# Kernel tuning notes

Measured on AMD Instinct MI355X. Metric: run time of the kernel, lower is better.

## Reference

```python
import jax, jax.numpy as jnp
import numpy as np

B, S, D = 1, 2048, 1024
NH, NKV, HD = 16, 4, 64
N_REP = NH // NKV


def _rope_tables(seq_len, half_dim, base=10000.0):
    inv_freq = 1.0 / (base ** (np.arange(0, half_dim, dtype=np.float32) / half_dim))
    t = np.arange(seq_len, dtype=np.float32)
    freqs = np.outer(t, inv_freq)  # (S, HD//2)
    return jnp.asarray(np.cos(freqs)), jnp.asarray(np.sin(freqs))


def setup_inputs() -> dict:
    key = jax.random.key(0)
    ks = jax.random.split(key, 5)
    x = jax.random.normal(ks[0], (B, S, D), dtype=jnp.float32)
    rope_cos, rope_sin = _rope_tables(S, HD // 2)
    sd = 1.0 / np.sqrt(D)
    Wq = jax.random.normal(ks[1], (D, NH * HD), dtype=jnp.float32) * sd
    Wk = jax.random.normal(ks[2], (D, NKV * HD), dtype=jnp.float32) * sd
    Wv = jax.random.normal(ks[3], (D, NKV * HD), dtype=jnp.float32) * sd
    Wo = jax.random.normal(ks[4], (NH * HD, D), dtype=jnp.float32) * sd
    return {"x": x, "rope_cos": rope_cos, "rope_sin": rope_sin,
            "Wq": Wq, "Wk": Wk, "Wv": Wv, "Wo": Wo}


def _apply_rope(t, cos, sin):
    # t: (B, H, S, HD); cos/sin: (S, HD//2). Rotate-half convention.
    t1, t2 = jnp.split(t, 2, axis=-1)
    c = cos[None, None, :, :]
    s = sin[None, None, :, :]
    return jnp.concatenate([t1 * c - t2 * s, t2 * c + t1 * s], axis=-1)


def reference(x, rope_cos, rope_sin, Wq, Wk, Wv, Wo):
    b, s, _ = x.shape
    # projections -> (B, H, S, HD)
    q = (x @ Wq).reshape(b, s, NH, HD).transpose(0, 2, 1, 3)
    k = (x @ Wk).reshape(b, s, NKV, HD).transpose(0, 2, 1, 3)
    v = (x @ Wv).reshape(b, s, NKV, HD).transpose(0, 2, 1, 3)
    q = _apply_rope(q, rope_cos, rope_sin)
    k = _apply_rope(k, rope_cos, rope_sin)
    # GQA expansion (repeat_interleave on head axis)
    k = jnp.repeat(k, N_REP, axis=1)
    v = jnp.repeat(v, N_REP, axis=1)
    scale = HD ** -0.5
    scores = jnp.einsum('bhqd,bhkd->bhqk', q, k) * scale
    causal = jnp.tril(jnp.ones((s, s), dtype=bool))
    scores = jnp.where(causal[None, None], scores, jnp.float32(-jnp.inf))
    attn = jax.nn.softmax(scores, axis=-1)
    out = jnp.einsum('bhqk,bhkd->bhqd', attn, v)  # (B, H, S, HD)
    out = out.transpose(0, 2, 1, 3).reshape(b, s, NH * HD)
    return out @ Wo
```

## Files before the change

kernel.cpp:

```cpp
#include <hip/hip_runtime.h>

typedef unsigned short ushort_t;
typedef __attribute__((ext_vector_type(8))) short short8;
typedef __attribute__((ext_vector_type(4))) float f32x4;
typedef __attribute__((ext_vector_type(4))) unsigned short ushort4v;
typedef __attribute__((ext_vector_type(8))) unsigned short ushort8v;

#define S_LEN 2048
#define D_MODEL 1024
#define NH 16
#define NKV 4
#define HD 64

__device__ __forceinline__ ushort_t f2bf(float f) {
    unsigned u = __float_as_uint(f);
    u += 0x7fffu + ((u >> 16) & 1u);
    return (ushort_t)(u >> 16);
}

__device__ __forceinline__ void cp16(void* lds, const void* g) {
    __builtin_amdgcn_global_load_lds(
        (__attribute__((address_space(1))) void*)g,
        (__attribute__((address_space(3))) void*)lds, 16, 0, 0);
}

__global__ __launch_bounds__(256) void prep_kernel(
    const float* __restrict__ x, ushort_t* __restrict__ xb,
    const float* __restrict__ Wq, const float* __restrict__ Wk,
    const float* __restrict__ Wv, const float* __restrict__ Wo,
    ushort_t* __restrict__ WqT, ushort_t* __restrict__ WkT,
    ushort_t* __restrict__ WvT, ushort_t* __restrict__ WoT)
{
    const int t = threadIdx.x;
    if (blockIdx.z == 4) {
        const int b  = blockIdx.y * 16 + blockIdx.x;
        const int i0 = (b * 256 + t) * 4;
        #pragma unroll
        for (int rep = 0; rep < 8; ++rep) {
            const int i = i0 + rep * 262144;
            float4 v = *(const float4*)(x + i);
            ushort4v o = { f2bf(v.x), f2bf(v.y), f2bf(v.z), f2bf(v.w) };
            *(ushort4v*)(xb + i) = o;
        }
        return;
    }
    __shared__ ushort_t T[64 * 72];
    const float* W; ushort_t* WT; int N;
    switch (blockIdx.z) {
        case 0:  W = Wq; WT = WqT; N = 1024; break;
        case 1:  W = Wk; WT = WkT; N = 256;  break;
        case 2:  W = Wv; WT = WvT; N = 256;  break;
        default: W = Wo; WT = WoT; N = 1024; break;
    }
    const int n0 = blockIdx.y * 64;
    if (n0 >= N) return;
    const int k0 = blockIdx.x * 64;
    const int kr = t >> 4, nc = (t & 15) * 4;
    #pragma unroll
    for (int p = 0; p < 4; ++p) {
        const int k = kr + p * 16;
        float4 v = *(const float4*)(W + (size_t)(k0 + k) * N + n0 + nc);
        T[(nc + 0) * 72 + k] = f2bf(v.x);
        T[(nc + 1) * 72 + k] = f2bf(v.y);
        T[(nc + 2) * 72 + k] = f2bf(v.z);
        T[(nc + 3) * 72 + k] = f2bf(v.w);
    }
    __syncthreads();
    const int n = t >> 2, seg = (t & 3) * 16;
    ushort8v a = *(ushort8v*)&T[n * 72 + seg];
    ushort8v b = *(ushort8v*)&T[n * 72 + seg + 8];
    *(ushort8v*)(WT + (size_t)(n0 + n) * 1024 + k0 + seg)     = a;
    *(ushort8v*)(WT + (size_t)(n0 + n) * 1024 + k0 + seg + 8) = b;
}

__global__ __launch_bounds__(256, 2) void gemm_qkv_mfma(
    const ushort_t* __restrict__ xb, const ushort_t* __restrict__ WqT,
    const ushort_t* __restrict__ WkT, const ushort_t* __restrict__ WvT,
    const float* __restrict__ rc, const float* __restrict__ rs,
    ushort_t* __restrict__ Qb, ushort_t* __restrict__ Kb,
    ushort_t* __restrict__ Vtb)
{
    __shared__ ushort_t As[2][64 * 64];
    __shared__ ushort_t Bs[2][128 * 64];

    const int t = threadIdx.x;
    const int lane = t & 63, wave = t >> 6;
    const int wr = wave >> 1, wc = wave & 1;
    const int quad = lane >> 4, l15 = lane & 15;
    const int lq = lane >> 3, lr = lane & 7;
    const int swz_st = (lr ^ lq) * 8;
    const int l7 = l15 & 7;
    const int fsw0 = (quad ^ l7) * 8;
    const int fsw1 = ((quad + 4) ^ l7) * 8;

    const int m0 = blockIdx.x * 64;
    const int cy = blockIdx.y;

    const ushort_t* WT; int nloc;
    if (cy < 8)       { WT = WqT; nloc = cy * 128; }
    else if (cy < 10) { WT = WkT; nloc = (cy - 8) * 128; }
    else              { WT = WvT; nloc = (cy - 10) * 128; }

    f32x4 acc[2][4];
    #pragma unroll
    for (int i = 0; i < 2; ++i)
        #pragma unroll
        for (int j = 0; j < 4; ++j) acc[i][j] = (f32x4)0.f;

    auto stage = [&](int buf, int k0) {
        #pragma unroll
        for (int i = 0; i < 2; ++i) {
            const int r = wave * 16 + i * 8 + lq;
            cp16(&As[buf][(wave * 16 + i * 8) * 64],
                 xb + (size_t)(m0 + r) * 1024 + k0 + swz_st);
        }
        #pragma unroll
        for (int i = 0; i < 4; ++i) {
            const int r = wave * 32 + i * 8 + lq;
            cp16(&Bs[buf][(wave * 32 + i * 8) * 64],
                 WT + (size_t)(nloc + r) * 1024 + k0 + swz_st);
        }
    };

    stage(0, 0);
    __syncthreads();

    for (int kk = 0; kk < 16; ++kk) {
        const int cur = kk & 1;
        if (kk + 1 < 16) stage(cur ^ 1, (kk + 1) * 64);

        const ushort_t* Ac = &As[cur][0];
        const ushort_t* Bc = &Bs[cur][0];
        #pragma unroll
        for (int hh = 0; hh < 2; ++hh) {
            const int fsw = hh ? fsw1 : fsw0;
            short8 av[2], bv[4];
            #pragma unroll
            for (int i = 0; i < 2; ++i)
                av[i] = *(const short8*)&Ac[(wr * 32 + i * 16 + l15) * 64 + fsw];
            #pragma unroll
            for (int j = 0; j < 4; ++j)
                bv[j] = *(const short8*)&Bc[(wc * 64 + j * 16 + l15) * 64 + fsw];
            #pragma unroll
            for (int i = 0; i < 2; ++i)
                #pragma unroll
                for (int j = 0; j < 4; ++j)
                    acc[i][j] = __builtin_amdgcn_mfma_f32_16x16x32_bf16(
                        av[i], bv[j], acc[i][j], 0, 0, 0);
        }
        __syncthreads();
    }

    if (cy < 10) {
        ushort_t* dst = (cy < 8) ? Qb : Kb;
        const float qs = (cy < 8) ? 0.125f : 1.0f;
        const int h = ((cy < 8) ? cy : (cy - 8)) * 2 + wc;
        #pragma unroll
        for (int i = 0; i < 2; ++i) {
            #pragma unroll
            for (int j = 0; j < 2; ++j) {
                const int d = j * 16 + l15;
                #pragma unroll
                for (int reg = 0; reg < 4; ++reg) {
                    const int s = m0 + wr * 32 + i * 16 + quad * 4 + reg;
                    const float c  = rc[s * 32 + d];
                    const float sn = rs[s * 32 + d];
                    const float v1 = acc[i][j][reg];
                    const float v2 = acc[i][j + 2][reg];
                    dst[((size_t)h * S_LEN + s) * HD + d]      = f2bf((v1 * c - v2 * sn) * qs);
                    dst[((size_t)h * S_LEN + s) * HD + d + 32] = f2bf((v2 * c + v1 * sn) * qs);
                }
            }
        }
    } else {
        const int vh = (cy - 10) * 2 + wc;
        #pragma unroll
        for (int i = 0; i < 2; ++i) {
            const int s0 = m0 + wr * 32 + i * 16 + quad * 4;
            #pragma unroll
            for (int j = 0; j < 4; ++j) {
                const int d = j * 16 + l15;
                ushort4v o = { f2bf(acc[i][j][0]), f2bf(acc[i][j][1]),
                               f2bf(acc[i][j][2]), f2bf(acc[i][j][3]) };
                *(ushort4v*)&Vtb[((size_t)vh * HD + d) * S_LEN + s0] = o;
            }
        }
    }
}

__global__ __launch_bounds__(128, 2) void attn_mfma(
    const ushort_t* __restrict__ Qb, const ushort_t* __restrict__ Kb,
    const ushort_t* __restrict__ Vtb, ushort_t* __restrict__ attnb)
{
    __shared__ ushort_t Ks[2][2][64 * 64];
    __shared__ ushort_t Vs[2][2][64 * 64];
    __shared__ ushort_t Ps[2][32 * 64];

    const int t = threadIdx.x;
    const int lane = t & 63, wave = t >> 6;
    const int quad = lane >> 4, l15 = lane & 15;
    const int lq = lane >> 3, lr = lane & 7;
    const int swz_st = (lr ^ lq) * 8;
    const int l7 = l15 & 7;
    const int fsw0 = (quad ^ l7) * 8;
    const int fsw1 = ((quad + 4) ^ l7) * 8;

    const int h  = blockIdx.x;
    const int y  = blockIdx.y;
    const int qt = (y < 16) ? y : 47 - y;
    const int q0 = qt * 64;
    const int kvh = h >> 2;
    const int wrow0 = q0 + wave * 32;

    const ushort_t* Qg = Qb + ((size_t)h * S_LEN + wrow0) * HD;
    const ushort_t* Kg = Kb + (size_t)kvh * S_LEN * HD;
    const ushort_t* Vg = Vtb + (size_t)kvh * HD * S_LEN;

    short8 aq[2][2];
    #pragma unroll
    for (int i = 0; i < 2; ++i) {
        aq[i][0] = *(const short8*)(Qg + (size_t)(i * 16 + l15) * HD + quad * 8);
        aq[i][1] = *(const short8*)(Qg + (size_t)(i * 16 + l15) * HD + 32 + quad * 8);
    }

    float ps[2][4];
    f32x4 Oacc[2][4];
    #pragma unroll
    for (int i = 0; i < 2; ++i)
        #pragma unroll
        for (int jb = 0; jb < 4; ++jb) { Oacc[i][jb] = (f32x4)0.f; ps[i][jb] = 0.f; }

    const int nround = (qt + 2) >> 1;

    auto stage = [&](int buf, int kvbase) {
        #pragma unroll
        for (int u = 0; u < 2; ++u)
            #pragma unroll
            for (int i = 0; i < 4; ++i) {
                const int r = wave * 32 + i * 8 + lq;
                cp16(&Ks[buf][u][(wave * 32 + i * 8) * 64],
                     Kg + (size_t)(kvbase + u * 64 + r) * 64 + swz_st);
                cp16(&Vs[buf][u][(wave * 32 + i * 8) * 64],
                     Vg + (size_t)r * 2048 + kvbase + u * 64 + swz_st);
            }
    };

    stage(0, 0);
    __syncthreads();

    ushort_t* Pw = &Ps[wave][0];

    for (int round = 0; round < nround; ++round) {
        const int cur = round & 1;
        if (round + 1 < nround) stage(cur ^ 1, (round + 1) * 128);

        #pragma unroll
        for (int u = 0; u < 2; ++u) {
            const int kv0 = round * 128 + u * 64;
            if (kv0 > q0 + 63) break;
            const ushort_t* Kc = &Ks[cur][u][0];
            const ushort_t* Vc = &Vs[cur][u][0];

            f32x4 sv[2][4];
            #pragma unroll
            for (int jb = 0; jb < 4; ++jb) {
                short8 b0 = *(const short8*)&Kc[(jb * 16 + l15) * 64 + fsw0];
                short8 b1 = *(const short8*)&Kc[(jb * 16 + l15) * 64 + fsw1];
                #pragma unroll
                for (int i = 0; i < 2; ++i) {
                    f32x4 z = (f32x4)0.f;
                    z = __builtin_amdgcn_mfma_f32_16x16x32_bf16(aq[i][0], b0, z, 0, 0, 0);
                    z = __builtin_amdgcn_mfma_f32_16x16x32_bf16(aq[i][1], b1, z, 0, 0, 0);
                    sv[i][jb] = z;
                }
            }

            const bool diag = (kv0 == q0);
            #pragma unroll
            for (int i = 0; i < 2; ++i)
                #pragma unroll
                for (int jb = 0; jb < 4; ++jb) {
                    const int col = kv0 + jb * 16 + l15;
                    #pragma unroll
                    for (int reg = 0; reg < 4; ++reg) {
                        float e = __expf(sv[i][jb][reg]);
                        if (diag && col > wrow0 + i * 16 + quad * 4 + reg) e = 0.f;
                        sv[i][jb][reg] = e;
                        ps[i][reg] += e;
                    }
                }

            #pragma unroll
            for (int i = 0; i < 2; ++i)
                #pragma unroll
                for (int jb = 0; jb < 4; ++jb)
                    #pragma unroll
                    for (int reg = 0; reg < 4; ++reg) {
                        const int row = i * 16 + quad * 4 + reg;
                        const int seg = (jb * 2 + (l15 >> 3)) ^ (row & 7);
                        Pw[row * 64 + seg * 8 + (l15 & 7)] =
                            (ushort_t)(__float_as_uint(sv[i][jb][reg]) >> 16);
                    }

            short8 pf[2][2];
            #pragma unroll
            for (int i = 0; i < 2; ++i) {
                pf[i][0] = *(const short8*)&Pw[(i * 16 + l15) * 64 + fsw0];
                pf[i][1] = *(const short8*)&Pw[(i * 16 + l15) * 64 + fsw1];
            }

            #pragma unroll
            for (int jb = 0; jb < 4; ++jb) {
                short8 v0 = *(const short8*)&Vc[(jb * 16 + l15) * 64 + fsw0];
                short8 v1 = *(const short8*)&Vc[(jb * 16 + l15) * 64 + fsw1];
                #pragma unroll
                for (int i = 0; i < 2; ++i) {
                    Oacc[i][jb] = __builtin_amdgcn_mfma_f32_16x16x32_bf16(
                        pf[i][0], v0, Oacc[i][jb], 0, 0, 0);
                    Oacc[i][jb] = __builtin_amdgcn_mfma_f32_16x16x32_bf16(
                        pf[i][1], v1, Oacc[i][jb], 0, 0, 0);
                }
            }
        }

        __syncthreads();
    }

    #pragma unroll
    for (int i = 0; i < 2; ++i)
        #pragma unroll
        for (int reg = 0; reg < 4; ++reg) {
            float l = ps[i][reg];
            l += __shfl_xor(l, 1);
            l += __shfl_xor(l, 2);
            l += __shfl_xor(l, 4);
            l += __shfl_xor(l, 8);
            const float inv = 1.f / l;
            const int s = wrow0 + i * 16 + quad * 4 + reg;
            #pragma unroll
            for (int jb = 0; jb < 4; ++jb)
                attnb[(size_t)s * D_MODEL + h * HD + jb * 16 + l15] =
                    f2bf(Oacc[i][jb][reg] * inv);
        }
}

__global__ __launch_bounds__(256, 2) void gemm_out_mfma(
    const ushort_t* __restrict__ Ab, const ushort_t* __restrict__ WoT,
    float* __restrict__ out)
{
    __shared__ ushort_t As[2][64 * 64];
    __shared__ ushort_t Bs[2][64 * 64];

    const int t = threadIdx.x;
    const int lane = t & 63, wave = t >> 6;
    const int wr = wave >> 1, wc = wave & 1;
    const int quad = lane >> 4, l15 = lane & 15;
    const int lq = lane >> 3, lr = lane & 7;
    const int swz_st = (lr ^ lq) * 8;
    const int l7 = l15 & 7;
    const int fsw0 = (quad ^ l7) * 8;
    const int fsw1 = ((quad + 4) ^ l7) * 8;

    const int m0 = blockIdx.x * 64;
    const int n0 = blockIdx.y * 64;

    f32x4 acc[2][2];
    #pragma unroll
    for (int i = 0; i < 2; ++i)
        #pragma unroll
        for (int j = 0; j < 2; ++j) acc[i][j] = (f32x4)0.f;

    auto stage = [&](int buf, int k0) {
        #pragma unroll
        for (int i = 0; i < 2; ++i) {
            const int r = wave * 16 + i * 8 + lq;
            cp16(&As[buf][(wave * 16 + i * 8) * 64],
                 Ab + (size_t)(m0 + r) * 1024 + k0 + swz_st);
            cp16(&Bs[buf][(wave * 16 + i * 8) * 64],
                 WoT + (size_t)(n0 + r) * 1024 + k0 + swz_st);
        }
    };

    stage(0, 0);
    __syncthreads();

    for (int kk = 0; kk < 16; ++kk) {
        const int cur = kk & 1;
        if (kk + 1 < 16) stage(cur ^ 1, (kk + 1) * 64);

        const ushort_t* Ac = &As[cur][0];
        const ushort_t* Bc = &Bs[cur][0];
        #pragma unroll
        for (int hh = 0; hh < 2; ++hh) {
            const int fsw = hh ? fsw1 : fsw0;
            short8 av[2], bv[2];
            #pragma unroll
            for (int i = 0; i < 2; ++i)
                av[i] = *(const short8*)&Ac[(wr * 32 + i * 16 + l15) * 64 + fsw];
            #pragma unroll
            for (int j = 0; j < 2; ++j)
                bv[j] = *(const short8*)&Bc[(wc * 32 + j * 16 + l15) * 64 + fsw];
            #pragma unroll
            for (int i = 0; i < 2; ++i)
                #pragma unroll
                for (int j = 0; j < 2; ++j)
                    acc[i][j] = __builtin_amdgcn_mfma_f32_16x16x32_bf16(
                        av[i], bv[j], acc[i][j], 0, 0, 0);
        }
        __syncthreads();
    }

    #pragma unroll
    for (int i = 0; i < 2; ++i)
        #pragma unroll
        for (int reg = 0; reg < 4; ++reg) {
            const int s = m0 + wr * 32 + i * 16 + quad * 4 + reg;
            #pragma unroll
            for (int j = 0; j < 2; ++j)
                out[(size_t)s * D_MODEL + n0 + wc * 32 + j * 16 + l15] = acc[i][j][reg];
        }
}

extern "C" void kernel_launch(void* const* d_in, const int* in_sizes, int n_in,
                              void* d_out, int out_size, void* d_ws, size_t ws_size,
                              hipStream_t stream)
{
    const float* x  = (const float*)d_in[0];
    const float* rc = (const float*)d_in[1];
    const float* rs = (const float*)d_in[2];
    const float* Wq = (const float*)d_in[3];
    const float* Wk = (const float*)d_in[4];
    const float* Wv = (const float*)d_in[5];
    const float* Wo = (const float*)d_in[6];
    float* out = (float*)d_out;

    ushort_t* xb   = (ushort_t*)d_ws;
    ushort_t* WqT  = xb   + (size_t)2048 * 1024;
    ushort_t* WkT  = WqT  + (size_t)1024 * 1024;
    ushort_t* WvT  = WkT  + (size_t)256 * 1024;
    ushort_t* WoT  = WvT  + (size_t)256 * 1024;
    ushort_t* Qb   = WoT  + (size_t)1024 * 1024;
    ushort_t* Kb   = Qb   + (size_t)NH * S_LEN * HD;
    ushort_t* Vtb  = Kb   + (size_t)NKV * S_LEN * HD;
    ushort_t* attnb= Vtb  + (size_t)NKV * HD * S_LEN;

    prep_kernel<<<dim3(16, 16, 5), 256, 0, stream>>>(x, xb, Wq, Wk, Wv, Wo,
                                                     WqT, WkT, WvT, WoT);
    gemm_qkv_mfma<<<dim3(32, 12), 256, 0, stream>>>(xb, WqT, WkT, WvT,
                                                    rc, rs, Qb, Kb, Vtb);
    attn_mfma<<<dim3(NH, 32), 128, 0, stream>>>(Qb, Kb, Vtb, attnb);
    gemm_out_mfma<<<dim3(32, 16), 256, 0, stream>>>(attnb, WoT, out);
}
```

Baseline: 154.4 us.

## Split causal attention along KV into partial blocks and add combine kernel

Attention work is now split along the KV axis (split-K / flash-decoding style). Each query tile is divided into up to four chunks of eight 64-wide KV tiles, giving 80×16 blocks with bounded work, launched longest-first. Partial unnormalized outputs and row sums are written in fp32 to a workspace, and a new combine kernel sums them, normalizes and converts to bf16. The goal is to balance the causal triangle's uneven load across CUs. The cost is extra fp32 global traffic, an extra kernel launch, and single-tile staging in place of 128-wide double tiles.

Result: faster. 146.5 us (-5.1%).

```diff
diff --git a/kernel.cpp b/kernel.cpp
--- a/kernel.cpp
+++ b/kernel.cpp
@@ -190,10 +190,11 @@
 
 __global__ __launch_bounds__(128, 2) void attn_mfma(
     const ushort_t* __restrict__ Qb, const ushort_t* __restrict__ Kb,
-    const ushort_t* __restrict__ Vtb, ushort_t* __restrict__ attnb)
-{
-    __shared__ ushort_t Ks[2][2][64 * 64];
-    __shared__ ushort_t Vs[2][2][64 * 64];
+    const ushort_t* __restrict__ Vtb, float* __restrict__ Opart,
+    float* __restrict__ lpart)
+{
+    __shared__ ushort_t Ks[2][64 * 64];
+    __shared__ ushort_t Vs[2][64 * 64];
     __shared__ ushort_t Ps[2][32 * 64];
 
     const int t = threadIdx.x;
@@ -205,10 +206,18 @@
     const int fsw0 = (quad ^ l7) * 8;
     const int fsw1 = ((quad + 4) ^ l7) * 8;
 
-    const int h  = blockIdx.x;
-    const int y  = blockIdx.y;
-    const int qt = (y < 16) ? y : 47 - y;
-    const int q0 = qt * 64;
+    const int x = 79 - blockIdx.x;
+    int qt, k;
+    if (x < 8)       { qt = x;               k = 0; }
+    else if (x < 24) { qt = 8 + (x - 8) / 2;  k = (x - 8) & 1; }
+    else if (x < 48) { qt = 16 + (x - 24) / 3; k = (x - 24) % 3; }
+    else             { qt = 24 + (x - 48) / 4; k = (x - 48) & 3; }
+    const int start = k * 8;
+    const int end   = min(start + 8, qt + 1);
+    const int nsub  = end - start;
+
+    const int h   = blockIdx.y;
+    const int q0  = qt * 64;
     const int kvh = h >> 2;
     const int wrow0 = q0 + wave * 32;
 
@@ -230,102 +239,98 @@
         #pragma unroll
         for (int jb = 0; jb < 4; ++jb) { Oacc[i][jb] = (f32x4)0.f; ps[i][jb] = 0.f; }
 
-    const int nround = (qt + 2) >> 1;
-
-    auto stage = [&](int buf, int kvbase) {
-        #pragma unroll
-        for (int u = 0; u < 2; ++u)
-            #pragma unroll
-            for (int i = 0; i < 4; ++i) {
-                const int r = wave * 32 + i * 8 + lq;
-                cp16(&Ks[buf][u][(wave * 32 + i * 8) * 64],
-                     Kg + (size_t)(kvbase + u * 64 + r) * 64 + swz_st);
-                cp16(&Vs[buf][u][(wave * 32 + i * 8) * 64],
-                     Vg + (size_t)r * 2048 + kvbase + u * 64 + swz_st);
+    auto stage = [&](int buf, int kvt) {
+        const int kvbase = kvt * 64;
+        #pragma unroll
+        for (int i = 0; i < 4; ++i) {
+            const int r = wave * 32 + i * 8 + lq;
+            cp16(&Ks[buf][(wave * 32 + i * 8) * 64],
+                 Kg + (size_t)(kvbase + r) * 64 + swz_st);
+            cp16(&Vs[buf][(wave * 32 + i * 8) * 64],
+                 Vg + (size_t)r * 2048 + kvbase + swz_st);
+        }
+    };
+
+    stage(0, start);
+    __syncthreads();
+
+    ushort_t* Pw = &Ps[wave][0];
+
+    for (int ssub = 0; ssub < nsub; ++ssub) {
+        const int cur = ssub & 1;
+        if (ssub + 1 < nsub) stage(cur ^ 1, start + ssub + 1);
+
+        const int kvt = start + ssub;
+        const int kv0 = kvt * 64;
+        const ushort_t* Kc = &Ks[cur][0];
+        const ushort_t* Vc = &Vs[cur][0];
+
+        f32x4 sv[2][4];
+        #pragma unroll
+        for (int jb = 0; jb < 4; ++jb) {
+            short8 b0 = *(const short8*)&Kc[(jb * 16 + l15) * 64 + fsw0];
+            short8 b1 = *(const short8*)&Kc[(jb * 16 + l15) * 64 + fsw1];
+            #pragma unroll
+            for (int i = 0; i < 2; ++i) {
+                f32x4 z = (f32x4)0.f;
+                z = __builtin_amdgcn_mfma_f32_16x16x32_bf16(aq[i][0], b0, z, 0, 0, 0);
+                z = __builtin_amdgcn_mfma_f32_16x16x32_bf16(aq[i][1], b1, z, 0, 0, 0);
+                sv[i][jb] = z;
             }
-    };
-
-    stage(0, 0);
-    __syncthreads();
-
-    ushort_t* Pw = &Ps[wave][0];
-
-    for (int round = 0; round < nround; ++round) {
-        const int cur = round & 1;
-        if (round + 1 < nround) stage(cur ^ 1, (round + 1) * 128);
-
-        #pragma unroll
-        for (int u = 0; u < 2; ++u) {
-            const int kv0 = round * 128 + u * 64;
-            if (kv0 > q0 + 63) break;
-            const ushort_t* Kc = &Ks[cur][u][0];
-            const ushort_t* Vc = &Vs[cur][u][0];
-
-            f32x4 sv[2][4];
+        }
+
+        const bool diag = (kvt == qt);
+        #pragma unroll
+        for (int i = 0; i < 2; ++i)
             #pragma unroll
             for (int jb = 0; jb < 4; ++jb) {
-                short8 b0 = *(const short8*)&Kc[(jb * 16 + l15) * 64 + fsw0];
-                short8 b1 = *(const short8*)&Kc[(jb * 16 + l15) * 64 + fsw1];
+                const int col = kv0 + jb * 16 + l15;
                 #pragma unroll
-                for (int i = 0; i < 2; ++i) {
-                    f32x4 z = (f32x4)0.f;
-                    z = __builtin_amdgcn_mfma_f32_16x16x32_bf16(aq[i][0], b0, z, 0, 0, 0);
-                    z = __builtin_amdgcn_mfma_f32_16x16x32_bf16(aq[i][1], b1, z, 0, 0, 0);
-                    sv[i][jb] = z;
+                for (int reg = 0; reg < 4; ++reg) {
+                    float e = __expf(sv[i][jb][reg]);
+                    if (diag && col > wrow0 + i * 16 + quad * 4 + reg) e = 0.f;
+                    sv[i][jb][reg] = e;
+                    ps[i][reg] += e;
                 }
             }
 
-            const bool diag = (kv0 == q0);
-            #pragma unroll
-            for (int i = 0; i < 2; ++i)
+        #pragma unroll
+        for (int i = 0; i < 2; ++i)
+            #pragma unroll
+            for (int jb = 0; jb < 4; ++jb)
                 #pragma unroll
-                for (int jb = 0; jb < 4; ++jb) {
-                    const int col = kv0 + jb * 16 + l15;
-                    #pragma unroll
-                    for (int reg = 0; reg < 4; ++reg) {
-                        float e = __expf(sv[i][jb][reg]);
-                        if (diag && col > wrow0 + i * 16 + quad * 4 + reg) e = 0.f;
-                        sv[i][jb][reg] = e;
-                        ps[i][reg] += e;
-                    }
+                for (int reg = 0; reg < 4; ++reg) {
+                    const int row = i * 16 + quad * 4 + reg;
+                    const int seg = (jb * 2 + (l15 >> 3)) ^ (row & 7);
+                    Pw[row * 64 + seg * 8 + (l15 & 7)] =
+                        (ushort_t)(__float_as_uint(sv[i][jb][reg]) >> 16);
                 }
 
-            #pragma unroll
-            for (int i = 0; i < 2; ++i)
-                #pragma unroll
-                for (int jb = 0; jb < 4; ++jb)
-                    #pragma unroll
-                    for (int reg = 0; reg < 4; ++reg) {
-                        const int row = i * 16 + quad * 4 + reg;
-                        const int seg = (jb * 2 + (l15 >> 3)) ^ (row & 7);
-                        Pw[row * 64 + seg * 8 + (l15 & 7)] =
-                            (ushort_t)(__float_as_uint(sv[i][jb][reg]) >> 16);
-                    }
-
-            short8 pf[2][2];
+        short8 pf[2][2];
+        #pragma unroll
+        for (int i = 0; i < 2; ++i) {
+            pf[i][0] = *(const short8*)&Pw[(i * 16 + l15) * 64 + fsw0];
+            pf[i][1] = *(const short8*)&Pw[(i * 16 + l15) * 64 + fsw1];
+        }
+
+        #pragma unroll
+        for (int jb = 0; jb < 4; ++jb) {
+            short8 v0 = *(const short8*)&Vc[(jb * 16 + l15) * 64 + fsw0];
+            short8 v1 = *(const short8*)&Vc[(jb * 16 + l15) * 64 + fsw1];
             #pragma unroll
             for (int i = 0; i < 2; ++i) {
-                pf[i][0] = *(const short8*)&Pw[(i * 16 + l15) * 64 + fsw0];
-                pf[i][1] = *(const short8*)&Pw[(i * 16 + l15) * 64 + fsw1];
+                Oacc[i][jb] = __builtin_amdgcn_mfma_f32_16x16x32_bf16(
+                    pf[i][0], v0, Oacc[i][jb], 0, 0, 0);
+                Oacc[i][jb] = __builtin_amdgcn_mfma_f32_16x16x32_bf16(
+                    pf[i][1], v1, Oacc[i][jb], 0, 0, 0);
             }
-
-            #pragma unroll
-            for (int jb = 0; jb < 4; ++jb) {
-                short8 v0 = *(const short8*)&Vc[(jb * 16 + l15) * 64 + fsw0];
-                short8 v1 = *(const short8*)&Vc[(jb * 16 + l15) * 64 + fsw1];
-                #pragma unroll
-                for (int i = 0; i < 2; ++i) {
-                    Oacc[i][jb] = __builtin_amdgcn_mfma_f32_16x16x32_bf16(
-                        pf[i][0], v0, Oacc[i][jb], 0, 0, 0);
-                    Oacc[i][jb] = __builtin_amdgcn_mfma_f32_16x16x32_bf16(
-                        pf[i][1], v1, Oacc[i][jb], 0, 0, 0);
-                }
-            }
         }
 
         __syncthreads();
     }
 
+    float* Op = Opart + (size_t)k * S_LEN * D_MODEL;
+    float* lp = lpart + (size_t)k * S_LEN * NH;
     #pragma unroll
     for (int i = 0; i < 2; ++i)
         #pragma unroll
@@ -335,13 +340,36 @@
             l += __shfl_xor(l, 2);
             l += __shfl_xor(l, 4);
             l += __shfl_xor(l, 8);
-            const float inv = 1.f / l;
             const int s = wrow0 + i * 16 + quad * 4 + reg;
+            if (l15 == 0) lp[s * NH + h] = l;
             #pragma unroll
             for (int jb = 0; jb < 4; ++jb)
-                attnb[(size_t)s * D_MODEL + h * HD + jb * 16 + l15] =
-                    f2bf(Oacc[i][jb][reg] * inv);
-        }
+                Op[(size_t)s * D_MODEL + h * HD + jb * 16 + l15] = Oacc[i][jb][reg];
+        }
+}
+
+__global__ __launch_bounds__(256) void attn_combine(
+    const float* __restrict__ Opart, const float* __restrict__ lpart,
+    ushort_t* __restrict__ attnb)
+{
+    const int s  = blockIdx.x;
+    const int qt = s >> 6;
+    const int nk = (qt >> 3) + 1;
+    const int c0 = threadIdx.x * 4;
+    const int h  = c0 >> 6;
+
+    float4 acc = *(const float4*)(Opart + (size_t)s * D_MODEL + c0);
+    float  l   = lpart[s * NH + h];
+    for (int k = 1; k < nk; ++k) {
+        float4 a = *(const float4*)(Opart + (size_t)k * S_LEN * D_MODEL
+                                    + (size_t)s * D_MODEL + c0);
+        acc.x += a.x; acc.y += a.y; acc.z += a.z; acc.w += a.w;
+        l += lpart[(size_t)k * S_LEN * NH + s * NH + h];
+    }
+    const float inv = 1.f / l;
+    ushort4v o = { f2bf(acc.x * inv), f2bf(acc.y * inv),
+                   f2bf(acc.z * inv), f2bf(acc.w * inv) };
+    *(ushort4v*)(attnb + (size_t)s * D_MODEL + c0) = o;
 }
 
 __global__ __launch_bounds__(256, 2) void gemm_out_mfma(
@@ -443,11 +471,14 @@
     ushort_t* Kb   = Qb   + (size_t)NH * S_LEN * HD;
     ushort_t* Vtb  = Kb   + (size_t)NKV * S_LEN * HD;
     ushort_t* attnb= Vtb  + (size_t)NKV * HD * S_LEN;
+    float* Opart = (float*)(attnb + (size_t)S_LEN * D_MODEL);
+    float* lpart = Opart + (size_t)4 * S_LEN * D_MODEL;
 
     prep_kernel<<<dim3(16, 16, 5), 256, 0, stream>>>(x, xb, Wq, Wk, Wv, Wo,
                                                      WqT, WkT, WvT, WoT);
     gemm_qkv_mfma<<<dim3(32, 12), 256, 0, stream>>>(xb, WqT, WkT, WvT,
                                                     rc, rs, Qb, Kb, Vtb);
-    attn_mfma<<<dim3(NH, 32), 128, 0, stream>>>(Qb, Kb, Vtb, attnb);
+    attn_mfma<<<dim3(80, NH), 128, 0, stream>>>(Qb, Kb, Vtb, Opart, lpart);
+    attn_combine<<<2048, 256, 0, stream>>>(Opart, lpart, attnb);
     gemm_out_mfma<<<dim3(32, 16), 256, 0, stream>>>(attnb, WoT, out);
 }
```
